# Optimization experiments

Measured on AMD Instinct MI355X. Metric: run time of the kernel, lower is better.

## Reference

```python
import jax, jax.numpy as jnp
import numpy as np

NUM_NODES = 500_000
HIDDEN = 256
OUT_DIM = 1
NUM_GRAPHS = 2048
NUM_EDGES = 1_000_000


def setup_inputs() -> dict:
    key = jax.random.key(0)
    ks = jax.random.split(key, 9)
    h_v = jax.random.normal(ks[0], (NUM_NODES, HIDDEN), dtype=jnp.float32)
    edge_index = jax.random.randint(ks[1], (2, NUM_EDGES), 0, NUM_NODES, dtype=jnp.int64)
    # guarantee every graph id appears at least once, then sort (PyG-style batch vector)
    rest = jax.random.randint(ks[2], (NUM_NODES - NUM_GRAPHS,), 0, NUM_GRAPHS, dtype=jnp.int64)
    batch = jnp.sort(jnp.concatenate([jnp.arange(NUM_GRAPHS, dtype=jnp.int64), rest]))
    s = 0.02
    W1 = jax.random.normal(ks[3], (HIDDEN, HIDDEN), dtype=jnp.float32) * s
    b1 = jnp.zeros((HIDDEN,), dtype=jnp.float32)
    W2 = jax.random.normal(ks[4], (HIDDEN, HIDDEN), dtype=jnp.float32) * s
    b2 = jnp.zeros((HIDDEN,), dtype=jnp.float32)
    W3 = jax.random.normal(ks[5], (HIDDEN, OUT_DIM), dtype=jnp.float32) * s
    b3 = jnp.zeros((OUT_DIM,), dtype=jnp.float32)
    return {"h_v": h_v, "edge_index": edge_index, "batch": batch,
            "W1": W1, "b1": b1, "W2": W2, "b2": b2, "W3": W3, "b3": b3}


def reference(h_v, edge_index, batch, W1, b1, W2, b2, W3, b3):
    # segment mean pooling over nodes grouped by graph id (nodes_with_edge is all-True)
    sums = jax.ops.segment_sum(h_v, batch, num_segments=NUM_GRAPHS)          # [G, H]
    counts = jax.ops.segment_sum(jnp.ones((h_v.shape[0],), h_v.dtype), batch,
                                 num_segments=NUM_GRAPHS)                     # [G]
    nonempty = counts > 0
    pooled = sums / jnp.maximum(counts, 1.0)[:, None]                         # [G, H]
    # 3-layer MLP (dropout is identity in eval mode)
    x = jax.nn.relu(pooled @ W1 + b1)
    x = jax.nn.relu(x @ W2 + b2)
    pred = x @ W3 + b3                                                        # [G, out_dim]
    # empty graphs emit zeros (as in the torch code); all ids present here anyway
    return jnp.where(nonempty[:, None], pred, 0.0)
```

## Files before the change

### kernel.cpp

```cpp
#include <hip/hip_runtime.h>

#define HIDDEN 256
#define NV4 (HIDDEN / 4)
#define GPB 4

typedef float f4 __attribute__((ext_vector_type(4)));

__device__ __forceinline__ int lower_bound_i(const int* __restrict__ a, int n, int v)
{
    int lo = 0, hi = n;
    while (lo < hi) {
        int mid = (lo + hi) >> 1;
        if (a[mid] < v) lo = mid + 1; else hi = mid;
    }
    return lo;
}

__device__ __forceinline__ f4 ntl(const f4* p) { return __builtin_nontemporal_load(p); }

#define LOAD8(X, base) do { \
    X##0 = ntl(p + (size_t)((base) + 0) * NV4); \
    X##1 = ntl(p + (size_t)((base) + 1) * NV4); \
    X##2 = ntl(p + (size_t)((base) + 2) * NV4); \
    X##3 = ntl(p + (size_t)((base) + 3) * NV4); \
    X##4 = ntl(p + (size_t)((base) + 4) * NV4); \
    X##5 = ntl(p + (size_t)((base) + 5) * NV4); \
    X##6 = ntl(p + (size_t)((base) + 6) * NV4); \
    X##7 = ntl(p + (size_t)((base) + 7) * NV4); \
} while (0)

#define ACC8(X) do { \
    a0 += X##0; a1 += X##1; a2 += X##2; a3 += X##3; \
    a0 += X##4; a1 += X##5; a2 += X##6; a3 += X##7; \
} while (0)

__global__ __launch_bounds__(512, 4) void fused_readout_kernel(
    const f4* __restrict__ hv4, const int* __restrict__ batch,
    const float* __restrict__ W1, const float* __restrict__ b1,
    const float* __restrict__ W2, const float* __restrict__ b2,
    const float* __restrict__ W3, const float* __restrict__ b3,
    float* __restrict__ out, int n_nodes, int n_graphs)
{
    const int t    = threadIdx.x;
    const int w    = t >> 6;
    const int lane = t & 63;
    const int a    = w >> 1;
    const int g    = blockIdx.x * GPB + a;

    __shared__ __align__(16) f4    part[8][64];
    __shared__ __align__(16) float xs[GPB][HIDDEN];
    __shared__ __align__(16) float ys[GPB][HIDDEN];
    __shared__ __align__(16) float zs[GPB][HIDDEN];
    __shared__ float scnt[GPB];

    int start = 0, end = 0;
    if (g < n_graphs) {
        start = lower_bound_i(batch, n_nodes, g);
        end   = (g + 1 < n_graphs) ? lower_bound_i(batch, n_nodes, g + 1)
                                   : n_nodes;
    }
    const int cnt  = end - start;
    const int half = (cnt + 1) >> 1;
    const int rs   = (w & 1) ? (start + half) : start;
    const int re   = (w & 1) ? end : (start + half);
    const int n    = re - rs;

    f4 a0 = (f4)0.f, a1 = (f4)0.f, a2 = (f4)0.f, a3 = (f4)0.f;
    f4 A0, A1, A2, A3, A4, A5, A6, A7;
    f4 B0, B1, B2, B3, B4, B5, B6, B7;

    const f4* p = hv4 + (size_t)rs * NV4 + lane;
    int i = 0;
    if (n >= 8) {
        LOAD8(A, 0);
        i = 8;
        for (; i + 16 <= n; i += 16) {
            LOAD8(B, i);     ACC8(A);
            LOAD8(A, i + 8); ACC8(B);
        }
        if (i + 8 <= n) { LOAD8(B, i); ACC8(A); i += 8; ACC8(B); }
        else            { ACC8(A); }
    }
    for (; i < n; ++i) a0 += ntl(p + (size_t)i * NV4);

    a0 += a1; a2 += a3; a0 += a2;
    part[w][lane] = a0;
    if ((w & 1) == 0 && lane == 0) scnt[a] = (float)cnt;
    __syncthreads();

    if (t < 256) {
        const int aa = t >> 6;
        const f4 p0 = part[2 * aa][lane], p1 = part[2 * aa + 1][lane];
        const float inv = 1.0f / fmaxf(scnt[aa], 1.0f);
        ((f4*)xs[aa])[lane] = (p0 + p1) * inv;
    }
    __syncthreads();

    const int tl = t & 255;
    const int ga = (t >> 8) * 2;
    const int gb = ga + 1;
    float accA, accB;

    accA = accB = b1[tl];
    for (int k = 0; k < HIDDEN; k += 8) {
        const float w0 = W1[(k + 0) * HIDDEN + tl];
        const float w1_ = W1[(k + 1) * HIDDEN + tl];
        const float w2_ = W1[(k + 2) * HIDDEN + tl];
        const float w3_ = W1[(k + 3) * HIDDEN + tl];
        const float w4 = W1[(k + 4) * HIDDEN + tl];
        const float w5 = W1[(k + 5) * HIDDEN + tl];
        const float w6 = W1[(k + 6) * HIDDEN + tl];
        const float w7 = W1[(k + 7) * HIDDEN + tl];
        const f4 xA0 = *(const f4*)&xs[ga][k];
        const f4 xA1 = *(const f4*)&xs[ga][k + 4];
        const f4 xB0 = *(const f4*)&xs[gb][k];
        const f4 xB1 = *(const f4*)&xs[gb][k + 4];
        accA = fmaf(xA0.x, w0, accA); accA = fmaf(xA0.y, w1_, accA);
        accA = fmaf(xA0.z, w2_, accA); accA = fmaf(xA0.w, w3_, accA);
        accA = fmaf(xA1.x, w4, accA); accA = fmaf(xA1.y, w5, accA);
        accA = fmaf(xA1.z, w6, accA); accA = fmaf(xA1.w, w7, accA);
        accB = fmaf(xB0.x, w0, accB); accB = fmaf(xB0.y, w1_, accB);
        accB = fmaf(xB0.z, w2_, accB); accB = fmaf(xB0.w, w3_, accB);
        accB = fmaf(xB1.x, w4, accB); accB = fmaf(xB1.y, w5, accB);
        accB = fmaf(xB1.z, w6, accB); accB = fmaf(xB1.w, w7, accB);
    }
    ys[ga][tl] = fmaxf(accA, 0.f);
    ys[gb][tl] = fmaxf(accB, 0.f);
    __syncthreads();

    accA = accB = b2[tl];
    for (int k = 0; k < HIDDEN; k += 8) {
        const float w0 = W2[(k + 0) * HIDDEN + tl];
        const float w1_ = W2[(k + 1) * HIDDEN + tl];
        const float w2_ = W2[(k + 2) * HIDDEN + tl];
        const float w3_ = W2[(k + 3) * HIDDEN + tl];
        const float w4 = W2[(k + 4) * HIDDEN + tl];
        const float w5 = W2[(k + 5) * HIDDEN + tl];
        const float w6 = W2[(k + 6) * HIDDEN + tl];
        const float w7 = W2[(k + 7) * HIDDEN + tl];
        const f4 xA0 = *(const f4*)&ys[ga][k];
        const f4 xA1 = *(const f4*)&ys[ga][k + 4];
        const f4 xB0 = *(const f4*)&ys[gb][k];
        const f4 xB1 = *(const f4*)&ys[gb][k + 4];
        accA = fmaf(xA0.x, w0, accA); accA = fmaf(xA0.y, w1_, accA);
        accA = fmaf(xA0.z, w2_, accA); accA = fmaf(xA0.w, w3_, accA);
        accA = fmaf(xA1.x, w4, accA); accA = fmaf(xA1.y, w5, accA);
        accA = fmaf(xA1.z, w6, accA); accA = fmaf(xA1.w, w7, accA);
        accB = fmaf(xB0.x, w0, accB); accB = fmaf(xB0.y, w1_, accB);
        accB = fmaf(xB0.z, w2_, accB); accB = fmaf(xB0.w, w3_, accB);
        accB = fmaf(xB1.x, w4, accB); accB = fmaf(xB1.y, w5, accB);
        accB = fmaf(xB1.z, w6, accB); accB = fmaf(xB1.w, w7, accB);
    }
    const float w3v = W3[tl];
    zs[ga][tl] = fmaxf(accA, 0.f) * w3v;
    zs[gb][tl] = fmaxf(accB, 0.f) * w3v;
    __syncthreads();

    if (w < 4) {
        const int gg = blockIdx.x * GPB + w;
        if (gg < n_graphs) {
            float r = zs[w][lane] + zs[w][64 + lane]
                    + zs[w][128 + lane] + zs[w][192 + lane];
            #pragma unroll
            for (int off = 32; off > 0; off >>= 1)
                r += __shfl_down(r, off, 64);
            if (lane == 0)
                out[gg] = (scnt[w] > 0.f) ? (r + b3[0]) : 0.f;
        }
    }
}

extern "C" void kernel_launch(void* const* d_in, const int* in_sizes, int n_in,
                              void* d_out, int out_size, void* d_ws, size_t ws_size,
                              hipStream_t stream) {
    const float* h_v  = (const float*)d_in[0];
    const int*   batch = (const int*)d_in[2];
    const float* W1 = (const float*)d_in[3];
    const float* b1 = (const float*)d_in[4];
    const float* W2 = (const float*)d_in[5];
    const float* b2 = (const float*)d_in[6];
    const float* W3 = (const float*)d_in[7];
    const float* b3 = (const float*)d_in[8];
    float* out = (float*)d_out;

    const int n_nodes  = in_sizes[2];
    const int n_graphs = out_size;

    const int nblocks = (n_graphs + GPB - 1) / GPB;
    fused_readout_kernel<<<nblocks, 512, 0, stream>>>(
        (const f4*)h_v, batch, W1, b1, W2, b2, W3, b3,
        out, n_nodes, n_graphs);
}
```

Baseline: 101.0 us.

## Assign one wave per graph and pack eight graphs per block

The number of graphs per block goes from 4 to 8, so each wavefront now reduces one whole graph instead of two waves splitting it. This drops the shared-memory partial-sum combine and one barrier. Each thread in the MLP now computes 4 graphs per weight load instead of 2, which halves the number of W1/W2 reads from global or cache memory across the grid. The trade-offs are half as many blocks (256), longer serial reduction chains per wave, and more registers per thread.

Result: slower. 103.5 us (+2.5%).

```diff
diff --git a/kernel.cpp b/kernel.cpp
--- a/kernel.cpp
+++ b/kernel.cpp
@@ -2,7 +2,7 @@
 
 #define HIDDEN 256
 #define NV4 (HIDDEN / 4)
-#define GPB 4
+#define GPB 8
 
 typedef float f4 __attribute__((ext_vector_type(4)));
 
@@ -44,10 +44,8 @@
     const int t    = threadIdx.x;
     const int w    = t >> 6;
     const int lane = t & 63;
-    const int a    = w >> 1;
-    const int g    = blockIdx.x * GPB + a;
+    const int g    = blockIdx.x * GPB + w;
 
-    __shared__ __align__(16) f4    part[8][64];
     __shared__ __align__(16) float xs[GPB][HIDDEN];
     __shared__ __align__(16) float ys[GPB][HIDDEN];
     __shared__ __align__(16) float zs[GPB][HIDDEN];
@@ -59,17 +57,14 @@
         end   = (g + 1 < n_graphs) ? lower_bound_i(batch, n_nodes, g + 1)
                                    : n_nodes;
     }
-    const int cnt  = end - start;
-    const int half = (cnt + 1) >> 1;
-    const int rs   = (w & 1) ? (start + half) : start;
-    const int re   = (w & 1) ? end : (start + half);
-    const int n    = re - rs;
+    const int cnt = end - start;
+    const int n   = cnt;
 
     f4 a0 = (f4)0.f, a1 = (f4)0.f, a2 = (f4)0.f, a3 = (f4)0.f;
     f4 A0, A1, A2, A3, A4, A5, A6, A7;
     f4 B0, B1, B2, B3, B4, B5, B6, B7;
 
-    const f4* p = hv4 + (size_t)rs * NV4 + lane;
+    const f4* p = hv4 + (size_t)start * NV4 + lane;
     int i = 0;
     if (n >= 8) {
         LOAD8(A, 0);
@@ -84,89 +79,63 @@
     for (; i < n; ++i) a0 += ntl(p + (size_t)i * NV4);
 
     a0 += a1; a2 += a3; a0 += a2;
-    part[w][lane] = a0;
-    if ((w & 1) == 0 && lane == 0) scnt[a] = (float)cnt;
-    __syncthreads();
-
-    if (t < 256) {
-        const int aa = t >> 6;
-        const f4 p0 = part[2 * aa][lane], p1 = part[2 * aa + 1][lane];
-        const float inv = 1.0f / fmaxf(scnt[aa], 1.0f);
-        ((f4*)xs[aa])[lane] = (p0 + p1) * inv;
-    }
+    const float inv = 1.0f / fmaxf((float)cnt, 1.0f);
+    ((f4*)xs[w])[lane] = a0 * inv;
+    if (lane == 0) scnt[w] = (float)cnt;
     __syncthreads();
 
     const int tl = t & 255;
-    const int ga = (t >> 8) * 2;
-    const int gb = ga + 1;
-    float accA, accB;
+    const int ga = (t >> 8) * 4;
+    float acc[4];
+    float wv[8];
 
-    accA = accB = b1[tl];
+    #pragma unroll
+    for (int j = 0; j < 4; ++j) acc[j] = b1[tl];
     for (int k = 0; k < HIDDEN; k += 8) {
-        const float w0 = W1[(k + 0) * HIDDEN + tl];
-        const float w1_ = W1[(k + 1) * HIDDEN + tl];
-        const float w2_ = W1[(k + 2) * HIDDEN + tl];
-        const float w3_ = W1[(k + 3) * HIDDEN + tl];
-        const float w4 = W1[(k + 4) * HIDDEN + tl];
-        const float w5 = W1[(k + 5) * HIDDEN + tl];
-        const float w6 = W1[(k + 6) * HIDDEN + tl];
-        const float w7 = W1[(k + 7) * HIDDEN + tl];
-        const f4 xA0 = *(const f4*)&xs[ga][k];
-        const f4 xA1 = *(const f4*)&xs[ga][k + 4];
-        const f4 xB0 = *(const f4*)&xs[gb][k];
-        const f4 xB1 = *(const f4*)&xs[gb][k + 4];
-        accA = fmaf(xA0.x, w0, accA); accA = fmaf(xA0.y, w1_, accA);
-        accA = fmaf(xA0.z, w2_, accA); accA = fmaf(xA0.w, w3_, accA);
-        accA = fmaf(xA1.x, w4, accA); accA = fmaf(xA1.y, w5, accA);
-        accA = fmaf(xA1.z, w6, accA); accA = fmaf(xA1.w, w7, accA);
-        accB = fmaf(xB0.x, w0, accB); accB = fmaf(xB0.y, w1_, accB);
-        accB = fmaf(xB0.z, w2_, accB); accB = fmaf(xB0.w, w3_, accB);
-        accB = fmaf(xB1.x, w4, accB); accB = fmaf(xB1.y, w5, accB);
-        accB = fmaf(xB1.z, w6, accB); accB = fmaf(xB1.w, w7, accB);
+        #pragma unroll
+        for (int u = 0; u < 8; ++u) wv[u] = W1[(k + u) * HIDDEN + tl];
+        #pragma unroll
+        for (int j = 0; j < 4; ++j) {
+            const f4 x0 = *(const f4*)&xs[ga + j][k];
+            const f4 x1 = *(const f4*)&xs[ga + j][k + 4];
+            acc[j] = fmaf(x0.x, wv[0], acc[j]); acc[j] = fmaf(x0.y, wv[1], acc[j]);
+            acc[j] = fmaf(x0.z, wv[2], acc[j]); acc[j] = fmaf(x0.w, wv[3], acc[j]);
+            acc[j] = fmaf(x1.x, wv[4], acc[j]); acc[j] = fmaf(x1.y, wv[5], acc[j]);
+            acc[j] = fmaf(x1.z, wv[6], acc[j]); acc[j] = fmaf(x1.w, wv[7], acc[j]);
+        }
     }
-    ys[ga][tl] = fmaxf(accA, 0.f);
-    ys[gb][tl] = fmaxf(accB, 0.f);
+    #pragma unroll
+    for (int j = 0; j < 4; ++j) ys[ga + j][tl] = fmaxf(acc[j], 0.f);
     __syncthreads();
 
-    accA = accB = b2[tl];
+    #pragma unroll
+    for (int j = 0; j < 4; ++j) acc[j] = b2[tl];
     for (int k = 0; k < HIDDEN; k += 8) {
-        const float w0 = W2[(k + 0) * HIDDEN + tl];
-        const float w1_ = W2[(k + 1) * HIDDEN + tl];
-        const float w2_ = W2[(k + 2) * HIDDEN + tl];
-        const float w3_ = W2[(k + 3) * HIDDEN + tl];
-        const float w4 = W2[(k + 4) * HIDDEN + tl];
-        const float w5 = W2[(k + 5) * HIDDEN + tl];
-        const float w6 = W2[(k + 6) * HIDDEN + tl];
-        const float w7 = W2[(k + 7) * HIDDEN + tl];
-        const f4 xA0 = *(const f4*)&ys[ga][k];
-        const f4 xA1 = *(const f4*)&ys[ga][k + 4];
-        const f4 xB0 = *(const f4*)&ys[gb][k];
-        const f4 xB1 = *(const f4*)&ys[gb][k + 4];
-        accA = fmaf(xA0.x, w0, accA); accA = fmaf(xA0.y, w1_, accA);
-        accA = fmaf(xA0.z, w2_, accA); accA = fmaf(xA0.w, w3_, accA);
-        accA = fmaf(xA1.x, w4, accA); accA = fmaf(xA1.y, w5, accA);
-        accA = fmaf(xA1.z, w6, accA); accA = fmaf(xA1.w, w7, accA);
-        accB = fmaf(xB0.x, w0, accB); accB = fmaf(xB0.y, w1_, accB);
-        accB = fmaf(xB0.z, w2_, accB); accB = fmaf(xB0.w, w3_, accB);
-        accB = fmaf(xB1.x, w4, accB); accB = fmaf(xB1.y, w5, accB);
-        accB = fmaf(xB1.z, w6, accB); accB = fmaf(xB1.w, w7, accB);
+        #pragma unroll
+        for (int u = 0; u < 8; ++u) wv[u] = W2[(k + u) * HIDDEN + tl];
+        #pragma unroll
+        for (int j = 0; j < 4; ++j) {
+            const f4 x0 = *(const f4*)&ys[ga + j][k];
+            const f4 x1 = *(const f4*)&ys[ga + j][k + 4];
+            acc[j] = fmaf(x0.x, wv[0], acc[j]); acc[j] = fmaf(x0.y, wv[1], acc[j]);
+            acc[j] = fmaf(x0.z, wv[2], acc[j]); acc[j] = fmaf(x0.w, wv[3], acc[j]);
+            acc[j] = fmaf(x1.x, wv[4], acc[j]); acc[j] = fmaf(x1.y, wv[5], acc[j]);
+            acc[j] = fmaf(x1.z, wv[6], acc[j]); acc[j] = fmaf(x1.w, wv[7], acc[j]);
+        }
     }
     const float w3v = W3[tl];
-    zs[ga][tl] = fmaxf(accA, 0.f) * w3v;
-    zs[gb][tl] = fmaxf(accB, 0.f) * w3v;
+    #pragma unroll
+    for (int j = 0; j < 4; ++j) zs[ga + j][tl] = fmaxf(acc[j], 0.f) * w3v;
     __syncthreads();
 
-    if (w < 4) {
-        const int gg = blockIdx.x * GPB + w;
-        if (gg < n_graphs) {
-            float r = zs[w][lane] + zs[w][64 + lane]
-                    + zs[w][128 + lane] + zs[w][192 + lane];
-            #pragma unroll
-            for (int off = 32; off > 0; off >>= 1)
-                r += __shfl_down(r, off, 64);
-            if (lane == 0)
-                out[gg] = (scnt[w] > 0.f) ? (r + b3[0]) : 0.f;
-        }
+    if (g < n_graphs) {
+        float r = zs[w][lane] + zs[w][64 + lane]
+                + zs[w][128 + lane] + zs[w][192 + lane];
+        #pragma unroll
+        for (int off = 32; off > 0; off >>= 1)
+            r += __shfl_down(r, off, 64);
+        if (lane == 0)
+            out[g] = (scnt[w] > 0.f) ? (r + b3[0]) : 0.f;
     }
 }
 
```
